# Performance work log

Measured on AMD Instinct MI355X. Metric: run time of the kernel, lower is better.

The kernel has to match this reference:

```python
import jax, jax.numpy as jnp
import numpy as np

THRESHOLD = 0.5
NEG_POS = 3
ALPHA = 1.0


def cxcy_to_xy(c):
    return jnp.concatenate([c[..., :2] - c[..., 2:] / 2, c[..., :2] + c[..., 2:] / 2], axis=-1)


def xy_to_cxcy(xy):
    return jnp.concatenate([(xy[..., :2] + xy[..., 2:]) / 2, xy[..., 2:] - xy[..., :2]], axis=-1)


def encode_bboxes(cxcy, priors_cxcy):
    # standard SSD encoding with variances (0.1, 0.2)
    return jnp.concatenate([
        (cxcy[..., :2] - priors_cxcy[..., :2]) / (priors_cxcy[..., 2:] / 10.0),
        jnp.log(cxcy[..., 2:] / priors_cxcy[..., 2:]) * 5.0,
    ], axis=-1)


def find_iou(b1, b2):
    # b1: [n,4] xy, b2: [m,4] xy -> [n,m]
    lt = jnp.maximum(b1[:, None, :2], b2[None, :, :2])
    rb = jnp.minimum(b1[:, None, 2:], b2[None, :, 2:])
    wh = jnp.clip(rb - lt, 0.0)
    inter = wh[..., 0] * wh[..., 1]
    a1 = (b1[:, 2] - b1[:, 0]) * (b1[:, 3] - b1[:, 1])
    a2 = (b2[:, 2] - b2[:, 0]) * (b2[:, 3] - b2[:, 1])
    return inter / (a1[:, None] + a2[None, :] - inter)


def setup_inputs() -> dict:
    key = jax.random.key(0)
    ks = jax.random.split(key, 6)
    B, D, C, O = 64, 8732, 81, 16
    locs_pred = jax.random.normal(ks[0], (B, D, 4), dtype=jnp.float32)
    cls_pred = jax.random.normal(ks[1], (B, D, C), dtype=jnp.float32)
    # valid gt boxes in xy format within [0,1]
    xy1 = jax.random.uniform(ks[2], (B, O, 2), dtype=jnp.float32) * 0.7
    wh = jax.random.uniform(ks[3], (B, O, 2), dtype=jnp.float32) * 0.25 + 0.05
    boxes = jnp.concatenate([xy1, xy1 + wh], axis=-1)
    labels = jax.random.randint(ks[4], (B, O), 1, C)
    # default boxes in cxcy format
    kc, kw = jax.random.split(ks[5])
    cxcy = jax.random.uniform(kc, (D, 2), dtype=jnp.float32)
    dwh = jax.random.uniform(kw, (D, 2), dtype=jnp.float32) * 0.3 + 0.05
    default_boxes = jnp.concatenate([cxcy, dwh], axis=-1)
    return {"locs_pred": locs_pred, "cls_pred": cls_pred, "boxes": boxes,
            "labels": labels, "default_boxes": default_boxes}


def _match_one(boxes_i, labels_i, default_boxes, default_boxes_xy):
    # boxes_i: [O,4] xy, labels_i: [O] int
    n_objects = boxes_i.shape[0]
    overlap = find_iou(boxes_i, default_boxes_xy)          # [O, D]
    overlap_each_def = overlap.max(axis=0)                  # [D]
    object_each_def = overlap.argmax(axis=0)                # [D]
    def_each_obj = overlap.argmax(axis=1)                   # [O]
    # force each object to be matched to its best default box
    object_each_def = object_each_def.at[def_each_obj].set(jnp.arange(n_objects))
    overlap_each_def = overlap_each_def.at[def_each_obj].set(1.0)
    label_each_def = labels_i[object_each_def]               # [D]
    label_each_def = jnp.where(overlap_each_def < THRESHOLD, 0, label_each_def)
    matched_cxcy = xy_to_cxcy(boxes_i[object_each_def])      # [D,4]
    target_loc = encode_bboxes(matched_cxcy, default_boxes)  # [D,4]
    return target_loc, label_each_def


def reference(locs_pred, cls_pred, boxes, labels, default_boxes):
    B, D, C = cls_pred.shape
    default_boxes_xy = cxcy_to_xy(default_boxes)
    target_locs, target_classes = jax.vmap(
        lambda b, l: _match_one(b, l, default_boxes, default_boxes_xy))(boxes, labels)
    # target_locs: [B,D,4], target_classes: [B,D]

    pos = target_classes != 0                                # [B,D]
    posf = pos.astype(locs_pred.dtype)
    n_positive = posf.sum(axis=1)                            # [B]
    n_pos_total = n_positive.sum()

    # SmoothL1 (beta=1), mean over positive elements (n_pos*4 elements)
    d = jnp.abs(locs_pred - target_locs)
    sl1 = jnp.where(d < 1.0, 0.5 * d * d, d - 0.5)           # [B,D,4]
    loc_loss = (sl1 * posf[..., None]).sum() / (n_pos_total * 4.0)

    # per-box cross entropy
    logp = jax.nn.log_softmax(cls_pred, axis=-1)             # [B,D,C]
    ce = -jnp.take_along_axis(logp, target_classes[..., None], axis=-1)[..., 0]  # [B,D]

    conf_pos_sum = (ce * posf).sum()
    neg_loss = jnp.where(pos, 0.0, ce)                       # [B,D]
    neg_sorted = -jnp.sort(-neg_loss, axis=1)                # descending
    n_hard_neg = NEG_POS * n_positive                        # [B]
    hard_mask = (jnp.arange(D)[None, :] < n_hard_neg[:, None]).astype(ce.dtype)
    conf_neg_sum = (neg_sorted * hard_mask).sum()
    conf_loss = (conf_neg_sum + conf_pos_sum) / n_pos_total

    return (ALPHA * loc_loss, conf_loss)
```

## Files before the change

kernel.cpp:

```cpp
#include <hip/hip_runtime.h>
#include <hip/hip_bf16.h>
#include <math.h>

#define MAXO 16
#define MWAVES 16

__global__ __launch_bounds__(1024, 1)
void match_kernel(const float* __restrict__ boxes,
                  const int*   __restrict__ labels,
                  const float* __restrict__ dboxes,
                  const float* __restrict__ locs,
                  int*    __restrict__ tcls,
                  int*    __restrict__ n_pos,
                  double* __restrict__ locpart,
                  int D, int O) {
    int b = blockIdx.x;
    int t = threadIdx.x;
    int nt = blockDim.x;

    extern __shared__ __align__(16) char smem[];
    float*         sOvl = (float*)smem;
    unsigned char* sObj = (unsigned char*)(smem + (size_t)D * 4);

    __shared__ float sbox[MAXO][4];
    __shared__ float sarea[MAXO];
    __shared__ int   slab[MAXO];
    __shared__ unsigned long long skey[MWAVES][MAXO];
    __shared__ int   sdstar[MAXO];
    __shared__ double sred[1024];
    __shared__ int    sredi[1024];

    if (t < O) {
        const float* bp = boxes + ((size_t)b * O + t) * 4;
        float x1 = bp[0], y1 = bp[1], x2 = bp[2], y2 = bp[3];
        sbox[t][0] = x1; sbox[t][1] = y1; sbox[t][2] = x2; sbox[t][3] = y2;
        sarea[t] = (x2 - x1) * (y2 - y1);
        slab[t]  = labels[(size_t)b * O + t];
    }
    __syncthreads();

    unsigned long long bestk[MAXO];
#pragma unroll
    for (int o = 0; o < MAXO; ++o) bestk[o] = 0ull;

    for (int d = t; d < D; d += nt) {
        float4 db = ((const float4*)dboxes)[d];
        float dx1 = db.x - db.z * 0.5f, dy1 = db.y - db.w * 0.5f;
        float dx2 = db.x + db.z * 0.5f, dy2 = db.y + db.w * 0.5f;
        float a2 = (dx2 - dx1) * (dy2 - dy1);
        unsigned notd = 0xFFFFFFFFu - (unsigned)d;
        float mval = -1.0f; int mobj = 0;
#pragma unroll
        for (int o = 0; o < MAXO; ++o) {
            if (o < O) {
                float lx = fmaxf(sbox[o][0], dx1), ly = fmaxf(sbox[o][1], dy1);
                float rx = fminf(sbox[o][2], dx2), ry = fminf(sbox[o][3], dy2);
                float w = fmaxf(rx - lx, 0.0f), h = fmaxf(ry - ly, 0.0f);
                float inter = w * h;
                float iou = inter / (sarea[o] + a2 - inter);
                if (iou > mval) { mval = iou; mobj = o; }
                unsigned long long key =
                    ((unsigned long long)__float_as_uint(iou) << 32) |
                    (unsigned long long)notd;
                if (key > bestk[o]) bestk[o] = key;
            }
        }
        sObj[d] = (unsigned char)mobj;
        sOvl[d] = mval;
    }

    int w = t >> 6;
#pragma unroll
    for (int o = 0; o < MAXO; ++o) {
        if (o < O) {
            unsigned long long k = bestk[o];
            for (int s = 32; s > 0; s >>= 1) {
                unsigned long long k2 =
                    (unsigned long long)__shfl_xor((long long)k, s);
                if (k2 > k) k = k2;
            }
            if ((t & 63) == 0) skey[w][o] = k;
        }
    }
    __syncthreads();
    if (t < O) {
        unsigned long long k = skey[0][t];
#pragma unroll
        for (int i = 1; i < MWAVES; ++i) {
            unsigned long long k2 = skey[i][t];
            if (k2 > k) k = k2;
        }
        sdstar[t] = (int)(0xFFFFFFFFu - (unsigned)(k & 0xFFFFFFFFull));
    }
    __syncthreads();

    double acc = 0.0;
    int cnt = 0;
    size_t rowoff = (size_t)b * D;
    for (int d = t; d < D; d += nt) {
        int o = sObj[d];
        float ov = sOvl[d];
#pragma unroll
        for (int oo = 0; oo < MAXO; ++oo) {
            if (oo < O && sdstar[oo] == d) { o = oo; ov = 1.0f; }
        }
        int lab = (ov < 0.5f) ? 0 : slab[o];
        tcls[rowoff + d] = lab;
        if (lab != 0) {
            cnt++;
            float x1 = sbox[o][0], y1 = sbox[o][1], x2 = sbox[o][2], y2 = sbox[o][3];
            float cx = (x1 + x2) * 0.5f, cy = (y1 + y2) * 0.5f;
            float w2 = x2 - x1, h2 = y2 - y1;
            float4 db = ((const float4*)dboxes)[d];
            float g0 = (cx - db.x) / (db.z * 0.1f);
            float g1 = (cy - db.y) / (db.w * 0.1f);
            float g2 = __logf(w2 / db.z) * 5.0f;
            float g3 = __logf(h2 / db.w) * 5.0f;
            float4 lp = ((const float4*)locs)[rowoff + d];
            float dd;
            dd = fabsf(lp.x - g0); acc += (dd < 1.0f) ? 0.5f * dd * dd : dd - 0.5f;
            dd = fabsf(lp.y - g1); acc += (dd < 1.0f) ? 0.5f * dd * dd : dd - 0.5f;
            dd = fabsf(lp.z - g2); acc += (dd < 1.0f) ? 0.5f * dd * dd : dd - 0.5f;
            dd = fabsf(lp.w - g3); acc += (dd < 1.0f) ? 0.5f * dd * dd : dd - 0.5f;
        }
    }
    sred[t] = acc; sredi[t] = cnt;
    __syncthreads();
    for (int s = 512; s > 0; s >>= 1) {
        if (t < s) { sred[t] += sred[t + s]; sredi[t] += sredi[t + s]; }
        __syncthreads();
    }
    if (t == 0) {
        n_pos[b]   = sredi[0];
        locpart[b] = sred[0];
    }
}

__global__ __launch_bounds__(256, 8)
void ce1p_kernel(const float* __restrict__ cls, const int* __restrict__ tcls,
                 float* __restrict__ negbuf, double* __restrict__ pospart,
                 int R) {
    int lane = threadIdx.x & 63;
    int p = lane & 3;
    int q = lane >> 2;
    int wid = (blockIdx.x * blockDim.x + threadIdx.x) >> 6;
    int nw  = (gridDim.x * blockDim.x) >> 6;
    double acc = 0.0;

    for (int base = wid * 16; base < R; base += nw * 16) {
        int row = base + q;
        bool valid = (row < R);
        const float* Ar = cls + (size_t)row * 81;
        const float* A  = Ar + p * 4;

        float e = 0.0f;
        if (valid) {
            float4 f0 = *(const float4*)(A);
            float4 f1 = *(const float4*)(A + 16);
            float4 f2 = *(const float4*)(A + 32);
            float4 f3 = *(const float4*)(A + 48);
            float4 f4 = *(const float4*)(A + 64);
            float e0 = __expf(f0.x) + __expf(f0.y) + __expf(f0.z) + __expf(f0.w);
            float e1 = __expf(f1.x) + __expf(f1.y) + __expf(f1.z) + __expf(f1.w);
            float e2 = __expf(f2.x) + __expf(f2.y) + __expf(f2.z) + __expf(f2.w);
            float e3 = __expf(f3.x) + __expf(f3.y) + __expf(f3.z) + __expf(f3.w);
            float e4 = __expf(f4.x) + __expf(f4.y) + __expf(f4.z) + __expf(f4.w);
            e = (e0 + e1) + (e2 + e3) + e4;
            if (p == 0) e += __expf(Ar[80]);
        }
        e += __shfl_xor(e, 1);
        e += __shfl_xor(e, 2);

        if (valid && p == 0) {
            int tgt = tcls[row];
            float lt = Ar[tgt];
            float ce = fmaxf(__logf(e) - lt, 0.0f);
            if (tgt != 0) { acc += (double)ce; negbuf[row] = 0.0f; }
            else          { negbuf[row] = ce; }
        }
    }

#pragma unroll
    for (int s = 4; s < 64; s <<= 1) acc += __shfl_xor(acc, s);
    __shared__ double swacc[4];
    if (lane == 0) swacc[threadIdx.x >> 6] = acc;
    __syncthreads();
    if (threadIdx.x == 0)
        pospart[blockIdx.x] = swacc[0] + swacc[1] + swacc[2] + swacc[3];
}

__global__ __launch_bounds__(256, 8)
void ce2_kernel(const float* __restrict__ cls, const int* __restrict__ tcls,
                float* __restrict__ negbuf, double* __restrict__ pospart,
                int R, int C) {
    int lane = threadIdx.x & 63;
    int wid  = (blockIdx.x * blockDim.x + threadIdx.x) >> 6;
    int nw   = (gridDim.x * blockDim.x) >> 6;
    double acc = 0.0;

    for (int r0 = wid * 2; r0 < R; r0 += nw * 2) {
        int r1 = r0 + 1;
        bool has1 = (r1 < R);
        const float* A  = cls + (size_t)r0 * C;
        const float* Bp = cls + (size_t)r1 * C;
        float a0 = (lane < C) ? A[lane] : -INFINITY;
        float a1 = (64 + lane < C) ? A[64 + lane] : -INFINITY;
        float b0 = (has1 && lane < C) ? Bp[lane] : -INFINITY;
        float b1 = (has1 && 64 + lane < C) ? Bp[64 + lane] : -INFINITY;
        int ta = tcls[r0];
        int tb = has1 ? tcls[r1] : 0;

        float ma = fmaxf(a0, a1), mb = fmaxf(b0, b1);
#pragma unroll
        for (int s = 32; s > 0; s >>= 1) {
            ma = fmaxf(ma, __shfl_xor(ma, s));
            mb = fmaxf(mb, __shfl_xor(mb, s));
        }
        float ea = __expf(a0 - ma) + __expf(a1 - ma);
        float eb = __expf(b0 - mb) + __expf(b1 - mb);
#pragma unroll
        for (int s = 32; s > 0; s >>= 1) {
            ea += __shfl_xor(ea, s);
            eb += __shfl_xor(eb, s);
        }
        int sa = (ta < 64) ? ta : ta - 64;
        int sb = (tb < 64) ? tb : tb - 64;
        float xa0 = __shfl(a0, sa), xa1 = __shfl(a1, sa);
        float xb0 = __shfl(b0, sb), xb1 = __shfl(b1, sb);
        float lta = (ta < 64) ? xa0 : xa1;
        float ltb = (tb < 64) ? xb0 : xb1;
        float cea = fmaxf(__logf(ea) + ma - lta, 0.0f);
        float ceb = fmaxf(__logf(eb) + mb - ltb, 0.0f);
        if (lane == 0) {
            if (ta != 0) { acc += (double)cea; negbuf[r0] = 0.0f; }
            else         { negbuf[r0] = cea; }
            if (has1) {
                if (tb != 0) { acc += (double)ceb; negbuf[r1] = 0.0f; }
                else         { negbuf[r1] = ceb; }
            }
        }
    }
    __shared__ double swacc[4];
    if (lane == 0) swacc[threadIdx.x >> 6] = acc;
    __syncthreads();
    if (threadIdx.x == 0)
        pospart[blockIdx.x] = swacc[0] + swacc[1] + swacc[2] + swacc[3];
}

__global__ __launch_bounds__(256) void hardneg_kernel(
        const float* __restrict__ neg, const int* __restrict__ n_pos,
        double* __restrict__ negpart, int D, int uselds) {
    extern __shared__ float ldsrow[];
    int b = blockIdx.x, t = threadIdx.x;
    int w = t >> 6;
    const float* row = neg + (size_t)b * D;

    __shared__ unsigned bins[4][256];
    __shared__ float    fbins[4][256];
    __shared__ unsigned sc[2][256];
    __shared__ float    sf[2][256];
    __shared__ unsigned sh_kk, sh_prefix, sh_pmask;
    __shared__ double   sh_above;

    int k0 = 3 * n_pos[b];
    if (k0 > D) k0 = D;
    if (t == 0) { sh_kk = (unsigned)k0; sh_prefix = 0u; sh_pmask = 0u; sh_above = 0.0; }
    __syncthreads();

    double tot = 0.0;
    if (k0 > 0) {
        for (int shift = 24; shift >= 0; shift -= 8) {
#pragma unroll
            for (int i = 0; i < 4; ++i) { bins[i][t] = 0; fbins[i][t] = 0.0f; }
            __syncthreads();
            unsigned pmask = sh_pmask, prefix = sh_prefix;
            unsigned kk = sh_kk;

            int      curbin = -1;
            unsigned ccnt = 0;
            float    csum = 0.0f;
            if (shift == 24) {
                for (int i = t; i < D; i += 256) {
                    float fv = row[i];
                    if (uselds) ldsrow[i] = fv;
                    unsigned v = __float_as_uint(fv);
                    int bin = (int)(v >> 24);
                    if (bin != curbin) {
                        if (ccnt) {
                            atomicAdd(&bins[w][curbin], ccnt);
                            atomicAdd(&fbins[w][curbin], csum);
                        }
                        curbin = bin; ccnt = 1; csum = fv;
                    } else { ccnt++; csum += fv; }
                }
            } else {
                for (int i = t; i < D; i += 256) {
                    float fv = uselds ? ldsrow[i] : row[i];
                    unsigned v = __float_as_uint(fv);
                    if ((v & pmask) == prefix) {
                        int bin = (int)((v >> shift) & 255u);
                        if (bin != curbin) {
                            if (ccnt) {
                                atomicAdd(&bins[w][curbin], ccnt);
                                atomicAdd(&fbins[w][curbin], csum);
                            }
                            curbin = bin; ccnt = 1; csum = fv;
                        } else { ccnt++; csum += fv; }
                    }
                }
            }
            if (ccnt) {
                atomicAdd(&bins[w][curbin], ccnt);
                atomicAdd(&fbins[w][curbin], csum);
            }
            __syncthreads();
            sc[0][t] = bins[0][t] + bins[1][t] + bins[2][t] + bins[3][t];
            sf[0][t] = fbins[0][t] + fbins[1][t] + fbins[2][t] + fbins[3][t];
            __syncthreads();
            int src = 0;
#pragma unroll
            for (int off = 1; off < 256; off <<= 1) {
                int dst = 1 - src;
                unsigned cv = sc[src][t] + ((t + off < 256) ? sc[src][t + off] : 0u);
                float    fv = sf[src][t] + ((t + off < 256) ? sf[src][t + off] : 0.0f);
                sc[dst][t] = cv; sf[dst][t] = fv;
                __syncthreads();
                src = dst;
            }
            unsigned sufc  = sc[src][t];
            unsigned above = (t < 255) ? sc[src][t + 1] : 0u;
            if (sufc >= kk && above < kk) {
                sh_above += (double)((t < 255) ? sf[src][t + 1] : 0.0f);
                sh_kk = kk - above;
                sh_prefix = prefix | ((unsigned)t << shift);
                sh_pmask = pmask | (255u << shift);
            }
            __syncthreads();
        }
        if (t == 0)
            tot = sh_above + (double)sh_kk * (double)__uint_as_float(sh_prefix);
    }
    if (t == 0) negpart[b] = tot;
}

__global__ void finalize_kernel(const double* __restrict__ locpart,
                                const double* __restrict__ pospart,
                                const double* __restrict__ negpart,
                                const int*    __restrict__ n_pos,
                                int B, int P, float* __restrict__ out) {
    __shared__ double sl[256], sp[256], sn[256];
    __shared__ int    si[256];
    int t = threadIdx.x;
    double l = 0.0, pp = 0.0, nn = 0.0; int c = 0;
    for (int i = t; i < B; i += 256) { l += locpart[i]; nn += negpart[i]; c += n_pos[i]; }
    for (int i = t; i < P; i += 256) pp += pospart[i];
    sl[t] = l; sp[t] = pp; sn[t] = nn; si[t] = c;
    __syncthreads();
    for (int s = 128; s > 0; s >>= 1) {
        if (t < s) { sl[t] += sl[t+s]; sp[t] += sp[t+s]; sn[t] += sn[t+s]; si[t] += si[t+s]; }
        __syncthreads();
    }
    if (t == 0) {
        double nd = (double)si[0];
        out[0] = (float)(sl[0] / (nd * 4.0));
        out[1] = (float)((sn[0] + sp[0]) / nd);
    }
}

extern "C" void kernel_launch(void* const* d_in, const int* in_sizes, int n_in,
                              void* d_out, int out_size, void* d_ws, size_t ws_size,
                              hipStream_t stream) {
    const float* locs   = (const float*)d_in[0];
    const float* cls    = (const float*)d_in[1];
    const float* boxes  = (const float*)d_in[2];
    const int*   labels = (const int*)d_in[3];
    const float* dboxes = (const float*)d_in[4];

    int D = in_sizes[4] / 4;
    int B = in_sizes[0] / (4 * D);
    int O = in_sizes[3] / B;
    int C = in_sizes[1] / (B * D);
    int R = B * D;
    const int NCE = 2048;

    char* ws = (char*)d_ws;
    size_t off = 0;
    double* locpart = (double*)(ws + off); off += (size_t)B * 8;
    double* negpart = (double*)(ws + off); off += (size_t)B * 8;
    double* pospart = (double*)(ws + off); off += (size_t)NCE * 8;
    int*    n_pos   = (int*)(ws + off);    off += (size_t)B * 4;
    off = (off + 15) & ~(size_t)15;
    int*    tcls    = (int*)(ws + off);    off += (size_t)R * 4;
    float*  negbuf  = (float*)(ws + off);

    size_t match_sh = (size_t)D * 4 + (size_t)D;
    match_kernel<<<B, 1024, match_sh, stream>>>(boxes, labels, dboxes, locs,
                                                tcls, n_pos, locpart, D, O);
    if (C == 81) {
        ce1p_kernel<<<NCE, 256, 0, stream>>>(cls, tcls, negbuf, pospart, R);
    } else {
        ce2_kernel<<<NCE, 256, 0, stream>>>(cls, tcls, negbuf, pospart, R, C);
    }
    int uselds = (D * 4 <= 40000) ? 1 : 0;
    size_t shbytes = uselds ? (size_t)D * 4 : 0;
    hardneg_kernel<<<B, 256, shbytes, stream>>>(negbuf, n_pos, negpart, D, uselds);
    finalize_kernel<<<1, 256, 0, stream>>>(locpart, pospart, negpart, n_pos,
                                           B, NCE, (float*)d_out);
}
```

Before: 127.3 us.

## Fold finalize into hardneg via last-block atomic and use one-pass CE grid

Removes the separate finalize kernel launch: each hardneg block bumps an atomic counter and the last block performs the final reduction, with the counter reset inside match_kernel. The CE kernel is relaunched with one 16-row tile per wave (grid sized to R/64 blocks) instead of a grid-stride loop over 2048 blocks. This trades a launch for fence/atomic overhead and enlarges the pospart array the final block must sum (~8.7k entries instead of 2048).

```diff
diff --git a/kernel.cpp b/kernel.cpp
--- a/kernel.cpp
+++ b/kernel.cpp
@@ -13,10 +13,13 @@
                   int*    __restrict__ tcls,
                   int*    __restrict__ n_pos,
                   double* __restrict__ locpart,
+                  int*    __restrict__ counter,
                   int D, int O) {
     int b = blockIdx.x;
     int t = threadIdx.x;
     int nt = blockDim.x;
+
+    if (b == 0 && t == 32) *counter = 0;
 
     extern __shared__ __align__(16) char smem[];
     float*         sOvl = (float*)smem;
@@ -144,40 +147,37 @@
     int p = lane & 3;
     int q = lane >> 2;
     int wid = (blockIdx.x * blockDim.x + threadIdx.x) >> 6;
-    int nw  = (gridDim.x * blockDim.x) >> 6;
     double acc = 0.0;
 
-    for (int base = wid * 16; base < R; base += nw * 16) {
-        int row = base + q;
-        bool valid = (row < R);
-        const float* Ar = cls + (size_t)row * 81;
-        const float* A  = Ar + p * 4;
-
-        float e = 0.0f;
-        if (valid) {
-            float4 f0 = *(const float4*)(A);
-            float4 f1 = *(const float4*)(A + 16);
-            float4 f2 = *(const float4*)(A + 32);
-            float4 f3 = *(const float4*)(A + 48);
-            float4 f4 = *(const float4*)(A + 64);
-            float e0 = __expf(f0.x) + __expf(f0.y) + __expf(f0.z) + __expf(f0.w);
-            float e1 = __expf(f1.x) + __expf(f1.y) + __expf(f1.z) + __expf(f1.w);
-            float e2 = __expf(f2.x) + __expf(f2.y) + __expf(f2.z) + __expf(f2.w);
-            float e3 = __expf(f3.x) + __expf(f3.y) + __expf(f3.z) + __expf(f3.w);
-            float e4 = __expf(f4.x) + __expf(f4.y) + __expf(f4.z) + __expf(f4.w);
-            e = (e0 + e1) + (e2 + e3) + e4;
-            if (p == 0) e += __expf(Ar[80]);
-        }
-        e += __shfl_xor(e, 1);
-        e += __shfl_xor(e, 2);
-
-        if (valid && p == 0) {
-            int tgt = tcls[row];
-            float lt = Ar[tgt];
-            float ce = fmaxf(__logf(e) - lt, 0.0f);
-            if (tgt != 0) { acc += (double)ce; negbuf[row] = 0.0f; }
-            else          { negbuf[row] = ce; }
-        }
+    int row = wid * 16 + q;
+    bool valid = (row < R);
+    const float* Ar = cls + (size_t)row * 81;
+    const float* A  = Ar + p * 4;
+
+    float e = 0.0f;
+    if (valid) {
+        float4 f0 = *(const float4*)(A);
+        float4 f1 = *(const float4*)(A + 16);
+        float4 f2 = *(const float4*)(A + 32);
+        float4 f3 = *(const float4*)(A + 48);
+        float4 f4 = *(const float4*)(A + 64);
+        float e0 = __expf(f0.x) + __expf(f0.y) + __expf(f0.z) + __expf(f0.w);
+        float e1 = __expf(f1.x) + __expf(f1.y) + __expf(f1.z) + __expf(f1.w);
+        float e2 = __expf(f2.x) + __expf(f2.y) + __expf(f2.z) + __expf(f2.w);
+        float e3 = __expf(f3.x) + __expf(f3.y) + __expf(f3.z) + __expf(f3.w);
+        float e4 = __expf(f4.x) + __expf(f4.y) + __expf(f4.z) + __expf(f4.w);
+        e = (e0 + e1) + (e2 + e3) + e4;
+        if (p == 0) e += __expf(Ar[80]);
+    }
+    e += __shfl_xor(e, 1);
+    e += __shfl_xor(e, 2);
+
+    if (valid && p == 0) {
+        int tgt = tcls[row];
+        float lt = Ar[tgt];
+        float ce = fmaxf(__logf(e) - lt, 0.0f);
+        if (tgt != 0) { acc = (double)ce; negbuf[row] = 0.0f; }
+        else          { negbuf[row] = ce; }
     }
 
 #pragma unroll
@@ -249,7 +249,10 @@
 
 __global__ __launch_bounds__(256) void hardneg_kernel(
         const float* __restrict__ neg, const int* __restrict__ n_pos,
-        double* __restrict__ negpart, int D, int uselds) {
+        double* __restrict__ negpart,
+        const double* __restrict__ locpart, const double* __restrict__ pospart,
+        int* __restrict__ counter, float* __restrict__ out,
+        int B, int P, int D, int uselds) {
     extern __shared__ float ldsrow[];
     int b = blockIdx.x, t = threadIdx.x;
     int w = t >> 6;
@@ -341,29 +344,33 @@
             tot = sh_above + (double)sh_kk * (double)__uint_as_float(sh_prefix);
     }
     if (t == 0) negpart[b] = tot;
-}
-
-__global__ void finalize_kernel(const double* __restrict__ locpart,
-                                const double* __restrict__ pospart,
-                                const double* __restrict__ negpart,
-                                const int*    __restrict__ n_pos,
-                                int B, int P, float* __restrict__ out) {
-    __shared__ double sl[256], sp[256], sn[256];
-    __shared__ int    si[256];
-    int t = threadIdx.x;
-    double l = 0.0, pp = 0.0, nn = 0.0; int c = 0;
-    for (int i = t; i < B; i += 256) { l += locpart[i]; nn += negpart[i]; c += n_pos[i]; }
-    for (int i = t; i < P; i += 256) pp += pospart[i];
-    sl[t] = l; sp[t] = pp; sn[t] = nn; si[t] = c;
-    __syncthreads();
-    for (int s = 128; s > 0; s >>= 1) {
-        if (t < s) { sl[t] += sl[t+s]; sp[t] += sp[t+s]; sn[t] += sn[t+s]; si[t] += si[t+s]; }
+
+    __threadfence();
+    __syncthreads();
+    __shared__ int slast;
+    if (t == 0) slast = atomicAdd(counter, 1);
+    __syncthreads();
+    if (slast == (int)gridDim.x - 1) {
+        __threadfence();
+        __shared__ double sl[256], sp[256], sn[256];
+        __shared__ int    si[256];
+        double l = 0.0, pp = 0.0, nn = 0.0; int c = 0;
+        for (int i = t; i < B; i += 256) {
+            l += locpart[i]; c += n_pos[i];
+            nn += *(volatile double*)&negpart[i];
+        }
+        for (int i = t; i < P; i += 256) pp += pospart[i];
+        sl[t] = l; sp[t] = pp; sn[t] = nn; si[t] = c;
         __syncthreads();
-    }
-    if (t == 0) {
-        double nd = (double)si[0];
-        out[0] = (float)(sl[0] / (nd * 4.0));
-        out[1] = (float)((sn[0] + sp[0]) / nd);
+        for (int s = 128; s > 0; s >>= 1) {
+            if (t < s) { sl[t] += sl[t+s]; sp[t] += sp[t+s]; sn[t] += sn[t+s]; si[t] += si[t+s]; }
+            __syncthreads();
+        }
+        if (t == 0) {
+            double nd = (double)si[0];
+            out[0] = (float)(sl[0] / (nd * 4.0));
+            out[1] = (float)((sn[0] + sp[0]) / nd);
+        }
     }
 }
 
@@ -381,29 +388,33 @@
     int O = in_sizes[3] / B;
     int C = in_sizes[1] / (B * D);
     int R = B * D;
-    const int NCE = 2048;
+
+    int nce = (R + 63) / 64;
+    const int NCE2 = 2048;
+    int P = (C == 81) ? nce : NCE2;
 
     char* ws = (char*)d_ws;
     size_t off = 0;
     double* locpart = (double*)(ws + off); off += (size_t)B * 8;
     double* negpart = (double*)(ws + off); off += (size_t)B * 8;
-    double* pospart = (double*)(ws + off); off += (size_t)NCE * 8;
+    double* pospart = (double*)(ws + off); off += (size_t)P * 8;
     int*    n_pos   = (int*)(ws + off);    off += (size_t)B * 4;
+    int*    counter = (int*)(ws + off);    off += 4;
     off = (off + 15) & ~(size_t)15;
     int*    tcls    = (int*)(ws + off);    off += (size_t)R * 4;
     float*  negbuf  = (float*)(ws + off);
 
     size_t match_sh = (size_t)D * 4 + (size_t)D;
     match_kernel<<<B, 1024, match_sh, stream>>>(boxes, labels, dboxes, locs,
-                                                tcls, n_pos, locpart, D, O);
+                                                tcls, n_pos, locpart, counter, D, O);
     if (C == 81) {
-        ce1p_kernel<<<NCE, 256, 0, stream>>>(cls, tcls, negbuf, pospart, R);
+        ce1p_kernel<<<nce, 256, 0, stream>>>(cls, tcls, negbuf, pospart, R);
     } else {
-        ce2_kernel<<<NCE, 256, 0, stream>>>(cls, tcls, negbuf, pospart, R, C);
+        ce2_kernel<<<NCE2, 256, 0, stream>>>(cls, tcls, negbuf, pospart, R, C);
     }
     int uselds = (D * 4 <= 40000) ? 1 : 0;
     size_t shbytes = uselds ? (size_t)D * 4 : 0;
-    hardneg_kernel<<<B, 256, shbytes, stream>>>(negbuf, n_pos, negpart, D, uselds);
-    finalize_kernel<<<1, 256, 0, stream>>>(locpart, pospart, negpart, n_pos,
-                                           B, NCE, (float*)d_out);
+    hardneg_kernel<<<B, 256, shbytes, stream>>>(negbuf, n_pos, negpart,
+                                                locpart, pospart, counter,
+                                                (float*)d_out, B, P, D, uselds);
 }
```

New measurement: 134.7 us. 1.06x slower.

## Fuse cross-entropy, hard-negative selection and finalize via last-block atomic counters

Applied to the files above, without the earlier changes.

The CE pass, the per-image hard-negative radix select and the final reduction are merged into one kernel. Each image's rows are split over 32 blocks, and the last block to finish (tracked with an atomic counter) runs the radix select for that image. The last image to finish then does the global finalize. This removes two kernel launches and their serialization gaps, and lets the hard-negative work overlap with CE blocks of other images. In exchange the select now runs on a single block late in the grid, reads negbuf from global memory (the LDS row cache is gone), and relies on threadfence and atomic ordering.

```diff
diff --git a/kernel.cpp b/kernel.cpp
--- a/kernel.cpp
+++ b/kernel.cpp
@@ -4,6 +4,7 @@
 
 #define MAXO 16
 #define MWAVES 16
+#define BPB 32
 
 __global__ __launch_bounds__(1024, 1)
 void match_kernel(const float* __restrict__ boxes,
@@ -13,10 +14,15 @@
                   int*    __restrict__ tcls,
                   int*    __restrict__ n_pos,
                   double* __restrict__ locpart,
+                  int*    __restrict__ cnt,
+                  int*    __restrict__ gcnt,
                   int D, int O) {
     int b = blockIdx.x;
     int t = threadIdx.x;
     int nt = blockDim.x;
+
+    if (t == 33) cnt[b] = 0;
+    if (b == 0 && t == 34) *gcnt = 0;
 
     extern __shared__ __align__(16) char smem[];
     float*         sOvl = (float*)smem;
@@ -95,7 +101,7 @@
     __syncthreads();
 
     double acc = 0.0;
-    int cnt = 0;
+    int cnt2 = 0;
     size_t rowoff = (size_t)b * D;
     for (int d = t; d < D; d += nt) {
         int o = sObj[d];
@@ -107,7 +113,7 @@
         int lab = (ov < 0.5f) ? 0 : slab[o];
         tcls[rowoff + d] = lab;
         if (lab != 0) {
-            cnt++;
+            cnt2++;
             float x1 = sbox[o][0], y1 = sbox[o][1], x2 = sbox[o][2], y2 = sbox[o][3];
             float cx = (x1 + x2) * 0.5f, cy = (y1 + y2) * 0.5f;
             float w2 = x2 - x1, h2 = y2 - y1;
@@ -124,7 +130,7 @@
             dd = fabsf(lp.w - g3); acc += (dd < 1.0f) ? 0.5f * dd * dd : dd - 0.5f;
         }
     }
-    sred[t] = acc; sredi[t] = cnt;
+    sred[t] = acc; sredi[t] = cnt2;
     __syncthreads();
     for (int s = 512; s > 0; s >>= 1) {
         if (t < s) { sred[t] += sred[t + s]; sredi[t] += sredi[t + s]; }
@@ -136,42 +142,54 @@
     }
 }
 
-__global__ __launch_bounds__(256, 8)
-void ce1p_kernel(const float* __restrict__ cls, const int* __restrict__ tcls,
-                 float* __restrict__ negbuf, double* __restrict__ pospart,
-                 int R) {
-    int lane = threadIdx.x & 63;
+__global__ __launch_bounds__(256)
+void ce_hn_kernel(const float* __restrict__ cls, const int* __restrict__ tcls,
+                  float* __restrict__ negbuf, double* __restrict__ pospart,
+                  const int* __restrict__ n_pos,
+                  const double* __restrict__ locpart,
+                  double* __restrict__ negpart,
+                  int* __restrict__ cnt, int* __restrict__ gcnt,
+                  float* __restrict__ out,
+                  int D, int B, int rows_pb) {
+    __shared__ unsigned bins[4][256];
+    __shared__ float    fbins[4][256];
+    __shared__ unsigned sc[2][256];
+    __shared__ float    sf[2][256];
+    __shared__ double   swacc[4];
+    __shared__ unsigned sh_kk, sh_prefix, sh_pmask;
+    __shared__ double   sh_above;
+    __shared__ int      sflag;
+
+    int blk = blockIdx.x;
+    int b = blk / BPB, qb = blk % BPB;
+    int tid = threadIdx.x;
+    int lane = tid & 63;
     int p = lane & 3;
-    int q = lane >> 2;
-    int wid = (blockIdx.x * blockDim.x + threadIdx.x) >> 6;
-    int nw  = (gridDim.x * blockDim.x) >> 6;
+    int qq = lane >> 2;
+    int wv = tid >> 6;
+
+    int rs = qb * rows_pb;
+    int re = rs + rows_pb; if (re > D) re = D;
     double acc = 0.0;
-
-    for (int base = wid * 16; base < R; base += nw * 16) {
-        int row = base + q;
-        bool valid = (row < R);
+    for (int ofs = rs + wv * 16 + qq; ofs < re; ofs += 64) {
+        int row = b * D + ofs;
         const float* Ar = cls + (size_t)row * 81;
         const float* A  = Ar + p * 4;
-
-        float e = 0.0f;
-        if (valid) {
-            float4 f0 = *(const float4*)(A);
-            float4 f1 = *(const float4*)(A + 16);
-            float4 f2 = *(const float4*)(A + 32);
-            float4 f3 = *(const float4*)(A + 48);
-            float4 f4 = *(const float4*)(A + 64);
-            float e0 = __expf(f0.x) + __expf(f0.y) + __expf(f0.z) + __expf(f0.w);
-            float e1 = __expf(f1.x) + __expf(f1.y) + __expf(f1.z) + __expf(f1.w);
-            float e2 = __expf(f2.x) + __expf(f2.y) + __expf(f2.z) + __expf(f2.w);
-            float e3 = __expf(f3.x) + __expf(f3.y) + __expf(f3.z) + __expf(f3.w);
-            float e4 = __expf(f4.x) + __expf(f4.y) + __expf(f4.z) + __expf(f4.w);
-            e = (e0 + e1) + (e2 + e3) + e4;
-            if (p == 0) e += __expf(Ar[80]);
-        }
+        float4 f0 = *(const float4*)(A);
+        float4 f1 = *(const float4*)(A + 16);
+        float4 f2 = *(const float4*)(A + 32);
+        float4 f3 = *(const float4*)(A + 48);
+        float4 f4 = *(const float4*)(A + 64);
+        float e0 = __expf(f0.x) + __expf(f0.y) + __expf(f0.z) + __expf(f0.w);
+        float e1 = __expf(f1.x) + __expf(f1.y) + __expf(f1.z) + __expf(f1.w);
+        float e2 = __expf(f2.x) + __expf(f2.y) + __expf(f2.z) + __expf(f2.w);
+        float e3 = __expf(f3.x) + __expf(f3.y) + __expf(f3.z) + __expf(f3.w);
+        float e4 = __expf(f4.x) + __expf(f4.y) + __expf(f4.z) + __expf(f4.w);
+        float e = (e0 + e1) + (e2 + e3) + e4;
+        if (p == 0) e += __expf(Ar[80]);
         e += __shfl_xor(e, 1);
         e += __shfl_xor(e, 2);
-
-        if (valid && p == 0) {
+        if (p == 0) {
             int tgt = tcls[row];
             float lt = Ar[tgt];
             float ce = fmaxf(__logf(e) - lt, 0.0f);
@@ -179,14 +197,113 @@
             else          { negbuf[row] = ce; }
         }
     }
-
 #pragma unroll
     for (int s = 4; s < 64; s <<= 1) acc += __shfl_xor(acc, s);
-    __shared__ double swacc[4];
-    if (lane == 0) swacc[threadIdx.x >> 6] = acc;
-    __syncthreads();
-    if (threadIdx.x == 0)
-        pospart[blockIdx.x] = swacc[0] + swacc[1] + swacc[2] + swacc[3];
+    if (lane == 0) swacc[wv] = acc;
+    __syncthreads();
+    if (tid == 0)
+        pospart[blk] = swacc[0] + swacc[1] + swacc[2] + swacc[3];
+
+    __threadfence();
+    if (tid == 0) sflag = (atomicAdd(&cnt[b], 1) == BPB - 1) ? 1 : 0;
+    __syncthreads();
+    if (!sflag) return;
+    __threadfence();
+
+    const float* row = negbuf + (size_t)b * D;
+    int w = wv;
+    int k0 = 3 * n_pos[b];
+    if (k0 > D) k0 = D;
+    if (tid == 0) { sh_kk = (unsigned)k0; sh_prefix = 0u; sh_pmask = 0u; sh_above = 0.0; }
+    __syncthreads();
+
+    double tot = 0.0;
+    if (k0 > 0) {
+        for (int shift = 24; shift >= 0; shift -= 8) {
+#pragma unroll
+            for (int i = 0; i < 4; ++i) { bins[i][tid] = 0; fbins[i][tid] = 0.0f; }
+            __syncthreads();
+            unsigned pmask = sh_pmask, prefix = sh_prefix;
+            unsigned kk = sh_kk;
+
+            int      curbin = -1;
+            unsigned ccnt = 0;
+            float    csum = 0.0f;
+            for (int i = tid; i < D; i += 256) {
+                float fv = row[i];
+                unsigned v = __float_as_uint(fv);
+                if ((v & pmask) == prefix) {
+                    int bin = (int)((v >> shift) & 255u);
+                    if (bin != curbin) {
+                        if (ccnt) {
+                            atomicAdd(&bins[w][curbin], ccnt);
+                            atomicAdd(&fbins[w][curbin], csum);
+                        }
+                        curbin = bin; ccnt = 1; csum = fv;
+                    } else { ccnt++; csum += fv; }
+                }
+            }
+            if (ccnt) {
+                atomicAdd(&bins[w][curbin], ccnt);
+                atomicAdd(&fbins[w][curbin], csum);
+            }
+            __syncthreads();
+            sc[0][tid] = bins[0][tid] + bins[1][tid] + bins[2][tid] + bins[3][tid];
+            sf[0][tid] = fbins[0][tid] + fbins[1][tid] + fbins[2][tid] + fbins[3][tid];
+            __syncthreads();
+            int src = 0;
+#pragma unroll
+            for (int off = 1; off < 256; off <<= 1) {
+                int dst = 1 - src;
+                unsigned cv = sc[src][tid] + ((tid + off < 256) ? sc[src][tid + off] : 0u);
+                float    fv = sf[src][tid] + ((tid + off < 256) ? sf[src][tid + off] : 0.0f);
+                sc[dst][tid] = cv; sf[dst][tid] = fv;
+                __syncthreads();
+                src = dst;
+            }
+            unsigned sufc  = sc[src][tid];
+            unsigned above = (tid < 255) ? sc[src][tid + 1] : 0u;
+            if (sufc >= kk && above < kk) {
+                sh_above += (double)((tid < 255) ? sf[src][tid + 1] : 0.0f);
+                sh_kk = kk - above;
+                sh_prefix = prefix | ((unsigned)tid << shift);
+                sh_pmask = pmask | (255u << shift);
+            }
+            __syncthreads();
+        }
+        if (tid == 0)
+            tot = sh_above + (double)sh_kk * (double)__uint_as_float(sh_prefix);
+    }
+    if (tid == 0) negpart[b] = tot;
+
+    __threadfence();
+    if (tid == 0) sflag = (atomicAdd(gcnt, 1) == B - 1) ? 1 : 0;
+    __syncthreads();
+    if (!sflag) return;
+    __threadfence();
+
+    double* sl = (double*)bins;
+    double* sp = (double*)fbins;
+    double* sn = (double*)sc;
+    int*    si = (int*)sf;
+    double l = 0.0, pp = 0.0, nn = 0.0; int c = 0;
+    int P = B * BPB;
+    for (int i = tid; i < B; i += 256) {
+        l += locpart[i]; nn += negpart[i]; c += n_pos[i];
+    }
+    for (int i = tid; i < P; i += 256) pp += pospart[i];
+    sl[tid] = l; sp[tid] = pp; sn[tid] = nn; si[tid] = c;
+    __syncthreads();
+    for (int s = 128; s > 0; s >>= 1) {
+        if (tid < s) { sl[tid] += sl[tid+s]; sp[tid] += sp[tid+s];
+                       sn[tid] += sn[tid+s]; si[tid] += si[tid+s]; }
+        __syncthreads();
+    }
+    if (tid == 0) {
+        double nd = (double)si[0];
+        out[0] = (float)(sl[0] / (nd * 4.0));
+        out[1] = (float)((sn[0] + sp[0]) / nd);
+    }
 }
 
 __global__ __launch_bounds__(256, 8)
@@ -249,8 +366,7 @@
 
 __global__ __launch_bounds__(256) void hardneg_kernel(
         const float* __restrict__ neg, const int* __restrict__ n_pos,
-        double* __restrict__ negpart, int D, int uselds) {
-    extern __shared__ float ldsrow[];
+        double* __restrict__ negpart, int D) {
     int b = blockIdx.x, t = threadIdx.x;
     int w = t >> 6;
     const float* row = neg + (size_t)b * D;
@@ -275,16 +391,14 @@
             __syncthreads();
             unsigned pmask = sh_pmask, prefix = sh_prefix;
             unsigned kk = sh_kk;
-
             int      curbin = -1;
             unsigned ccnt = 0;
             float    csum = 0.0f;
-            if (shift == 24) {
-                for (int i = t; i < D; i += 256) {
-                    float fv = row[i];
-                    if (uselds) ldsrow[i] = fv;
-                    unsigned v = __float_as_uint(fv);
-                    int bin = (int)(v >> 24);
+            for (int i = t; i < D; i += 256) {
+                float fv = row[i];
+                unsigned v = __float_as_uint(fv);
+                if ((v & pmask) == prefix) {
+                    int bin = (int)((v >> shift) & 255u);
                     if (bin != curbin) {
                         if (ccnt) {
                             atomicAdd(&bins[w][curbin], ccnt);
@@ -292,21 +406,6 @@
                         }
                         curbin = bin; ccnt = 1; csum = fv;
                     } else { ccnt++; csum += fv; }
-                }
-            } else {
-                for (int i = t; i < D; i += 256) {
-                    float fv = uselds ? ldsrow[i] : row[i];
-                    unsigned v = __float_as_uint(fv);
-                    if ((v & pmask) == prefix) {
-                        int bin = (int)((v >> shift) & 255u);
-                        if (bin != curbin) {
-                            if (ccnt) {
-                                atomicAdd(&bins[w][curbin], ccnt);
-                                atomicAdd(&fbins[w][curbin], csum);
-                            }
-                            curbin = bin; ccnt = 1; csum = fv;
-                        } else { ccnt++; csum += fv; }
-                    }
                 }
             }
             if (ccnt) {
@@ -381,29 +480,37 @@
     int O = in_sizes[3] / B;
     int C = in_sizes[1] / (B * D);
     int R = B * D;
-    const int NCE = 2048;
+
+    int P = B * BPB;
+    const int NCE2 = 2048;
+    if (C != 81 && NCE2 > P) P = NCE2;
 
     char* ws = (char*)d_ws;
     size_t off = 0;
     double* locpart = (double*)(ws + off); off += (size_t)B * 8;
     double* negpart = (double*)(ws + off); off += (size_t)B * 8;
-    double* pospart = (double*)(ws + off); off += (size_t)NCE * 8;
+    double* pospart = (double*)(ws + off); off += (size_t)P * 8;
     int*    n_pos   = (int*)(ws + off);    off += (size_t)B * 4;
+    int*    cnt     = (int*)(ws + off);    off += (size_t)B * 4;
+    int*    gcnt    = (int*)(ws + off);    off += 4;
     off = (off + 15) & ~(size_t)15;
     int*    tcls    = (int*)(ws + off);    off += (size_t)R * 4;
     float*  negbuf  = (float*)(ws + off);
 
     size_t match_sh = (size_t)D * 4 + (size_t)D;
     match_kernel<<<B, 1024, match_sh, stream>>>(boxes, labels, dboxes, locs,
-                                                tcls, n_pos, locpart, D, O);
+                                                tcls, n_pos, locpart, cnt, gcnt,
+                                                D, O);
     if (C == 81) {
-        ce1p_kernel<<<NCE, 256, 0, stream>>>(cls, tcls, negbuf, pospart, R);
+        int rows_pb = (D + BPB - 1) / BPB;
+        ce_hn_kernel<<<B * BPB, 256, 0, stream>>>(cls, tcls, negbuf, pospart,
+                                                  n_pos, locpart, negpart,
+                                                  cnt, gcnt, (float*)d_out,
+                                                  D, B, rows_pb);
     } else {
-        ce2_kernel<<<NCE, 256, 0, stream>>>(cls, tcls, negbuf, pospart, R, C);
-    }
-    int uselds = (D * 4 <= 40000) ? 1 : 0;
-    size_t shbytes = uselds ? (size_t)D * 4 : 0;
-    hardneg_kernel<<<B, 256, shbytes, stream>>>(negbuf, n_pos, negpart, D, uselds);
-    finalize_kernel<<<1, 256, 0, stream>>>(locpart, pospart, negpart, n_pos,
-                                           B, NCE, (float*)d_out);
+        ce2_kernel<<<NCE2, 256, 0, stream>>>(cls, tcls, negbuf, pospart, R, C);
+        hardneg_kernel<<<B, 256, 0, stream>>>(negbuf, n_pos, negpart, D);
+        finalize_kernel<<<1, 256, 0, stream>>>(locpart, pospart, negpart, n_pos,
+                                               B, NCE2, (float*)d_out);
+    }
 }
```

New measurement: 438.3 us. +244.2%, slower.
